# Optimization experiments

Measured on AMD Instinct MI355X. Metric: run time of the kernel, lower is better.

## Reference

```python
import jax, jax.numpy as jnp
import numpy as np

N = 100000   # num nodes
E = 1200000  # num edges
D = 64       # hidden_channel == middle_channel
ALPHA = 0.5
LN_EPS = 1e-5


def setup_inputs() -> dict:
    key = jax.random.key(0)
    ks = jax.random.split(key, 8)
    z = jax.random.normal(ks[0], (N, D), jnp.float32)
    x = jax.random.normal(ks[1], (N, D), jnp.float32)
    edge_index = jax.random.randint(ks[2], (2, E), 0, N)
    norm_factor = jax.random.uniform(ks[3], (N, 1), jnp.float32)  # >0 a.s.
    s = 0.1
    W = jax.random.normal(ks[4], (D, D), jnp.float32) * s    # nn.Linear(hidden, hidden, bias=False).weight
    U_w = jax.random.normal(ks[5], (D, D), jnp.float32) * s  # nn.Linear(hidden, middle).weight
    U_b = jax.random.normal(ks[6], (D,), jnp.float32) * s    # nn.Linear(hidden, middle).bias
    ln_gamma = jnp.ones((D,), jnp.float32)
    ln_beta = jnp.zeros((D,), jnp.float32)
    return dict(z=z, x=x, edge_index=edge_index, norm_factor=norm_factor,
                W=W, U_w=U_w, U_b=U_b, ln_gamma=ln_gamma, ln_beta=ln_beta)


def reference(z, x, edge_index, norm_factor, W, U_w, U_b, ln_gamma, ln_beta):
    row, col = edge_index[0], edge_index[1]
    # rescale=True: degree = 1/norm_factor with inf -> 0 (safe division)
    safe_nf = jnp.where(norm_factor > 0, norm_factor, 1.0)
    degree = jnp.where(norm_factor > 0, 1.0 / safe_nf, 0.0)  # [N,1]
    # double_linear=True: W(z) + degree * U(x), then graph-norm scale
    WzUx = z @ W.T + degree * (x @ U_w.T + U_b)  # [N,D]
    WzUx = norm_factor * WzUx
    # edge diff (gather), act + LayerNorm (batch=None path)
    e = WzUx[row] - WzUx[col]                    # [E,D]
    e = jax.nn.relu(e)
    mu = jnp.mean(e, axis=-1, keepdims=True)
    var = jnp.var(e, axis=-1, keepdims=True)
    e = (e - mu) * jax.lax.rsqrt(var + LN_EPS) * ln_gamma + ln_beta
    # double scatter_add aggregation
    new_z = jax.ops.segment_sum(e * norm_factor[row], row, num_segments=N)
    new_z = new_z - jax.ops.segment_sum(e * norm_factor[col], col, num_segments=N)
    # -F.linear(new_z, W.t()) == -(new_z @ W)
    new_z = -(new_z @ W)
    # dropout p=0.0 -> identity
    return ALPHA * new_z + (1.0 - ALPHA) * z
```

## Files before the change

### kernel.cpp

```cpp
#include <hip/hip_runtime.h>

#define D 64
#define LN_EPS 1e-5f
#define ALPHA 0.5f

#define GSH 8
#define GBN 256
#define NSUB 8
#define TILE 2048
#define CAPS 1280
#define CAPQ 1792
#define OVF_CAP 131072
#define MAXBUCK 400

__device__ __forceinline__ unsigned xcc_id() {
    unsigned v;
    asm volatile("s_getreg_b32 %0, hwreg(HW_REG_XCC_ID)" : "=s"(v));
    return v & (NSUB - 1);
}

__global__ __launch_bounds__(256) void wzux_kernel(
    const float* __restrict__ z, const float* __restrict__ x,
    const float* __restrict__ nf, const float* __restrict__ W,
    const float* __restrict__ Uw, const float* __restrict__ Ub,
    float* __restrict__ wzux, int N)
{
    const int lane = threadIdx.x & 63;
    const int wid  = threadIdx.x >> 6;
    const int par  = blockIdx.x & 1;
    const int half = lane >> 5;
    const int d    = par * 32 + (lane & 31);

    const float* M = half ? Uw : W;
    float4 wreg[16];
    {
        const float4* wr = (const float4*)(M + (size_t)d * D);
#pragma unroll
        for (int i = 0; i < 16; ++i) wreg[i] = wr[i];
    }
    const float ub = Ub[d];
    const float* base_src = half ? x : z;

    const int start = (blockIdx.x >> 1) * 4 + wid;
    const int step  = (gridDim.x >> 1) * 4;

    for (int n = start; n < N; n += step) {
        const int un = __builtin_amdgcn_readfirstlane(n);
        const float4* src = (const float4*)(base_src + (size_t)un * D);
        float a0 = 0.f, a1 = 0.f, a2 = 0.f, a3 = 0.f;
#pragma unroll
        for (int c = 0; c < 16; ++c) {
            float4 v = src[c];
            a0 = fmaf(v.x, wreg[c].x, a0);
            a1 = fmaf(v.y, wreg[c].y, a1);
            a2 = fmaf(v.z, wreg[c].z, a2);
            a3 = fmaf(v.w, wreg[c].w, a3);
        }
        float acc = (a0 + a1) + (a2 + a3);
        float other = __shfl_xor(acc, 32);
        if (half == 0) {
            float nfv = nf[un];
            float deg = (nfv > 0.f) ? (1.f / nfv) : 0.f;
            wzux[(size_t)un * D + d] = nfv * (acc + deg * (other + ub));
        }
    }
}

__global__ __launch_bounds__(256) void radix_scatter_kernel(
    const int* __restrict__ row, const int* __restrict__ col,
    int* __restrict__ gcur, int* __restrict__ data,
    int* __restrict__ ovf_cnt, int2* __restrict__ ovf,
    int E, int nbuck)
{
    __shared__ int cnt[MAXBUCK];
    __shared__ int gbase[MAXBUCK];
    const int t  = threadIdx.x;
    const int e0 = blockIdx.x * TILE;
    const int e1 = min(e0 + TILE, E);
    const unsigned sub = xcc_id();

    for (int i = t; i < nbuck; i += 256) cnt[i] = 0;
    __syncthreads();

    for (int e = e0 + t; e < e1; e += 256) {
        atomicAdd(&cnt[row[e] >> GSH], 1);
        atomicAdd(&cnt[col[e] >> GSH], 1);
    }
    __syncthreads();

    for (int b = t; b < nbuck; b += 256) {
        int c = cnt[b];
        gbase[b] = (c > 0) ? atomicAdd(&gcur[b * NSUB + sub], c) : 0;
    }
    __syncthreads();

    for (int e = e0 + t; e < e1; e += 256) {
        int r = row[e], c = col[e];
        {
            int b = r >> GSH;
            int s = atomicSub(&cnt[b], 1) - 1;
            int pos = gbase[b] + s;
            int rec = (c << 9) | ((r & (GBN - 1)) << 1);
            if (pos < CAPS) data[(b * NSUB + (int)sub) * CAPS + pos] = rec;
            else { int o = atomicAdd(ovf_cnt, 1);
                   if (o < OVF_CAP) ovf[o] = make_int2(b, rec); }
        }
        {
            int b = c >> GSH;
            int s = atomicSub(&cnt[b], 1) - 1;
            int pos = gbase[b] + s;
            int rec = (r << 9) | ((c & (GBN - 1)) << 1) | 1;
            if (pos < CAPS) data[(b * NSUB + (int)sub) * CAPS + pos] = rec;
            else { int o = atomicAdd(ovf_cnt, 1);
                   if (o < OVF_CAP) ovf[o] = make_int2(b, rec); }
        }
    }
}

__global__ __launch_bounds__(256) void bucket_sort_agg_kernel(
    const float4* __restrict__ wzux4,
    const int* __restrict__ gcur, const int* __restrict__ data,
    const int* __restrict__ ovf_cnt, const int2* __restrict__ ovf,
    const float* __restrict__ nf,
    const float4* __restrict__ gamma4, const float4* __restrict__ beta4,
    float4* __restrict__ out4, int N)
{
    __shared__ int sorted[CAPQ];
    __shared__ int offs[65];
    __shared__ int curs[64];

    const int blk    = blockIdx.x;
    const int base   = blk << 6;
    const int cntN   = min(64, N - base);
    const int bucket = blk >> 2;
    const int q      = blk & 3;
    const int t      = threadIdx.x;

    if (t < 65) offs[t] = 0;
    __syncthreads();

    const int ocnt = min(*ovf_cnt, OVF_CAP);

    for (int sub = 0; sub < NSUB; ++sub) {
        const int cs = min(gcur[bucket * NSUB + sub], CAPS);
        const int* p = &data[(bucket * NSUB + sub) * CAPS];
        for (int i = t; i < cs; i += 256) {
            int l8 = (p[i] >> 1) & (GBN - 1);
            if ((l8 >> 6) == q) atomicAdd(&offs[(l8 & 63) + 1], 1);
        }
    }
    for (int i = t; i < ocnt; i += 256) {
        int2 v = ovf[i];
        int l8 = (v.y >> 1) & (GBN - 1);
        if (v.x == bucket && (l8 >> 6) == q) atomicAdd(&offs[(l8 & 63) + 1], 1);
    }
    __syncthreads();

    if (t < 64) {
        int v = offs[t + 1];
#pragma unroll
        for (int off = 1; off < 64; off <<= 1) {
            int u = __shfl_up(v, off);
            if (t >= off) v += u;
        }
        offs[t + 1] = v;
    }
    __syncthreads();
    if (t < 64) curs[t] = offs[t];
    __syncthreads();

    for (int sub = 0; sub < NSUB; ++sub) {
        const int cs = min(gcur[bucket * NSUB + sub], CAPS);
        const int* p = &data[(bucket * NSUB + sub) * CAPS];
        for (int i = t; i < cs; i += 256) {
            int rec = p[i];
            int l8 = (rec >> 1) & (GBN - 1);
            if ((l8 >> 6) == q) {
                int pos = atomicAdd(&curs[l8 & 63], 1);
                if (pos < CAPQ) sorted[pos] = rec;
            }
        }
    }
    for (int i = t; i < ocnt; i += 256) {
        int2 v = ovf[i];
        int l8 = (v.y >> 1) & (GBN - 1);
        if (v.x == bucket && (l8 >> 6) == q) {
            int pos = atomicAdd(&curs[l8 & 63], 1);
            if (pos < CAPQ) sorted[pos] = v.y;
        }
    }
    __syncthreads();

    const int lane = t & 63;
    const int wid  = t >> 6;
    const int g = lane >> 4;
    const int l = lane & 15;
    const float4 gm = gamma4[l];
    const float4 bt = beta4[l];

    for (int local = wid; local < cntN; local += 4) {
        const int s = min(offs[local], CAPQ);
        const int e = min(offs[local + 1], CAPQ);
        const int n = base + local;
        const float4 self = wzux4[n * 16 + l];
        float4 acc = make_float4(0.f, 0.f, 0.f, 0.f);

#define PROC2(ENT, OROW)                                                     \
        {                                                                    \
            int ent = (ENT);                                                 \
            float sgn = (ent & 1) ? -1.f : 1.f;                              \
            float4 o = (OROW);                                               \
            float r0 = fmaxf(sgn * (self.x - o.x), 0.f);                     \
            float r1 = fmaxf(sgn * (self.y - o.y), 0.f);                     \
            float r2 = fmaxf(sgn * (self.z - o.z), 0.f);                     \
            float r3 = fmaxf(sgn * (self.w - o.w), 0.f);                     \
            float ss = r0 + r1 + r2 + r3;                                    \
            float sq = r0 * r0 + r1 * r1 + r2 * r2 + r3 * r3;                \
            _Pragma("unroll")                                                \
            for (int off = 1; off < 16; off <<= 1) {                         \
                ss += __shfl_xor(ss, off);                                   \
                sq += __shfl_xor(sq, off);                                   \
            }                                                                \
            float mu   = ss * (1.f / 64.f);                                  \
            float var  = sq * (1.f / 64.f) - mu * mu;                        \
            float rstd = rsqrtf(var + LN_EPS);                               \
            acc.x += sgn * ((r0 - mu) * rstd * gm.x + bt.x);                 \
            acc.y += sgn * ((r1 - mu) * rstd * gm.y + bt.y);                 \
            acc.z += sgn * ((r2 - mu) * rstd * gm.z + bt.z);                 \
            acc.w += sgn * ((r3 - mu) * rstd * gm.w + bt.w);                 \
        }

        int i = s + g;
        for (; i + 4 < e; i += 8) {
            int ea = sorted[i];
            int eb = sorted[i + 4];
            float4 oa = wzux4[(ea >> 9) * 16 + l];
            float4 ob = wzux4[(eb >> 9) * 16 + l];
            PROC2(ea, oa);
            PROC2(eb, ob);
        }
        if (i < e) {
            int ea = sorted[i];
            float4 oa = wzux4[(ea >> 9) * 16 + l];
            PROC2(ea, oa);
        }
#undef PROC2

#pragma unroll
        for (int m = 16; m < 64; m <<= 1) {
            acc.x += __shfl_xor(acc.x, m);
            acc.y += __shfl_xor(acc.y, m);
            acc.z += __shfl_xor(acc.z, m);
            acc.w += __shfl_xor(acc.w, m);
        }

        if (g == 0) {
            float nfv = nf[n];
            out4[n * 16 + l] = make_float4(acc.x * nfv, acc.y * nfv,
                                           acc.z * nfv, acc.w * nfv);
        }
    }
}

__global__ __launch_bounds__(256) void out_kernel(
    const float* accv, const float* __restrict__ z,
    const float* __restrict__ W, float* out, int N)
{
    const int lane = threadIdx.x & 63;
    const int wid  = threadIdx.x >> 6;

    float wcol[D];
#pragma unroll
    for (int k = 0; k < D; ++k) wcol[k] = W[k * D + lane];

    for (int n = blockIdx.x * 4 + wid; n < N; n += gridDim.x * 4) {
        const int un = __builtin_amdgcn_readfirstlane(n);
        const float4* ar = (const float4*)(accv + (size_t)un * D);
        float a0 = 0.f, a1 = 0.f, a2 = 0.f, a3 = 0.f;
#pragma unroll
        for (int c = 0; c < 16; ++c) {
            float4 a = ar[c];
            a0 = fmaf(a.x, wcol[c * 4 + 0], a0);
            a1 = fmaf(a.y, wcol[c * 4 + 1], a1);
            a2 = fmaf(a.z, wcol[c * 4 + 2], a2);
            a3 = fmaf(a.w, wcol[c * 4 + 3], a3);
        }
        float acc = (a0 + a1) + (a2 + a3);
        out[(size_t)un * D + lane] =
            (1.0f - ALPHA) * z[(size_t)un * D + lane] - ALPHA * acc;
    }
}

extern "C" void kernel_launch(void* const* d_in, const int* in_sizes, int n_in,
                              void* d_out, int out_size, void* d_ws, size_t ws_size,
                              hipStream_t stream) {
    const float* z     = (const float*)d_in[0];
    const float* x     = (const float*)d_in[1];
    const int*   ei    = (const int*)d_in[2];
    const float* nf    = (const float*)d_in[3];
    const float* W     = (const float*)d_in[4];
    const float* Uw    = (const float*)d_in[5];
    const float* Ub    = (const float*)d_in[6];
    const float* gamma = (const float*)d_in[7];
    const float* beta  = (const float*)d_in[8];

    const int N = in_sizes[0] / D;
    const int E = in_sizes[2] / 2;
    const int nbuck = (N + GBN - 1) >> GSH;

    float* out = (float*)d_out;

    char* ws = (char*)d_ws;
    size_t off = 0;
    auto alloc = [&](size_t bytes) {
        char* p = ws + off;
        off += (bytes + 255) & ~(size_t)255;
        return p;
    };
    float* wzux    = (float*)alloc((size_t)N * D * sizeof(float));
    int*   gcur    = (int*)  alloc((size_t)nbuck * NSUB * sizeof(int));
    int*   ovf_cnt = (int*)  alloc(sizeof(int));
    int*   data    = (int*)  alloc((size_t)nbuck * NSUB * CAPS * sizeof(int));
    int2*  ovf     = (int2*) alloc((size_t)OVF_CAP * sizeof(int2));

    hipMemsetAsync(gcur, 0, (size_t)nbuck * NSUB * sizeof(int), stream);
    hipMemsetAsync(ovf_cnt, 0, sizeof(int), stream);

    wzux_kernel<<<2048, 256, 0, stream>>>(z, x, nf, W, Uw, Ub, wzux, N);

    int sb = (E + TILE - 1) / TILE;
    radix_scatter_kernel<<<sb, 256, 0, stream>>>(ei, ei + E, gcur, data,
                                                 ovf_cnt, ovf, E, nbuck);

    int ab = (N + 63) / 64;
    bucket_sort_agg_kernel<<<ab, 256, 0, stream>>>(
        (const float4*)wzux, gcur, data, ovf_cnt, ovf, nf,
        (const float4*)gamma, (const float4*)beta,
        (float4*)out, N);

    out_kernel<<<2048, 256, 0, stream>>>(out, z, W, out, N);
}
```

Before: 341.4 us.

## Merge independent front kernels and fuse output GEMV into aggregation

The wzux linear-projection kernel and the radix edge-scatter kernel are independent, so they are merged into one launch, with block ranges dispatched to each role so both run concurrently. The final out_kernel (new_z @ W plus residual) is fused into the aggregation kernel. Each wave stages its reduced row in shared memory and computes the 64x64 matvec with W columns held in registers. This removes two launches and a global round trip of the intermediate row, at the cost of 64 extra registers per thread in the aggregation kernel, which may lower occupancy.

```diff
diff --git a/kernel.cpp b/kernel.cpp
--- a/kernel.cpp
+++ b/kernel.cpp
@@ -12,6 +12,7 @@
 #define CAPQ 1792
 #define OVF_CAP 131072
 #define MAXBUCK 400
+#define WZB 2048
 
 __device__ __forceinline__ unsigned xcc_id() {
     unsigned v;
@@ -19,100 +20,101 @@
     return v & (NSUB - 1);
 }
 
-__global__ __launch_bounds__(256) void wzux_kernel(
+__global__ __launch_bounds__(256) void front_kernel(
+    const int* __restrict__ row, const int* __restrict__ col,
+    int* __restrict__ gcur, int* __restrict__ data,
+    int* __restrict__ ovf_cnt, int2* __restrict__ ovf,
+    int E, int nbuck, int sb,
     const float* __restrict__ z, const float* __restrict__ x,
     const float* __restrict__ nf, const float* __restrict__ W,
     const float* __restrict__ Uw, const float* __restrict__ Ub,
     float* __restrict__ wzux, int N)
 {
-    const int lane = threadIdx.x & 63;
-    const int wid  = threadIdx.x >> 6;
-    const int par  = blockIdx.x & 1;
-    const int half = lane >> 5;
-    const int d    = par * 32 + (lane & 31);
-
-    const float* M = half ? Uw : W;
-    float4 wreg[16];
-    {
-        const float4* wr = (const float4*)(M + (size_t)d * D);
-#pragma unroll
-        for (int i = 0; i < 16; ++i) wreg[i] = wr[i];
-    }
-    const float ub = Ub[d];
-    const float* base_src = half ? x : z;
-
-    const int start = (blockIdx.x >> 1) * 4 + wid;
-    const int step  = (gridDim.x >> 1) * 4;
-
-    for (int n = start; n < N; n += step) {
-        const int un = __builtin_amdgcn_readfirstlane(n);
-        const float4* src = (const float4*)(base_src + (size_t)un * D);
-        float a0 = 0.f, a1 = 0.f, a2 = 0.f, a3 = 0.f;
-#pragma unroll
-        for (int c = 0; c < 16; ++c) {
-            float4 v = src[c];
-            a0 = fmaf(v.x, wreg[c].x, a0);
-            a1 = fmaf(v.y, wreg[c].y, a1);
-            a2 = fmaf(v.z, wreg[c].z, a2);
-            a3 = fmaf(v.w, wreg[c].w, a3);
-        }
-        float acc = (a0 + a1) + (a2 + a3);
-        float other = __shfl_xor(acc, 32);
-        if (half == 0) {
-            float nfv = nf[un];
-            float deg = (nfv > 0.f) ? (1.f / nfv) : 0.f;
-            wzux[(size_t)un * D + d] = nfv * (acc + deg * (other + ub));
-        }
-    }
-}
-
-__global__ __launch_bounds__(256) void radix_scatter_kernel(
-    const int* __restrict__ row, const int* __restrict__ col,
-    int* __restrict__ gcur, int* __restrict__ data,
-    int* __restrict__ ovf_cnt, int2* __restrict__ ovf,
-    int E, int nbuck)
-{
     __shared__ int cnt[MAXBUCK];
     __shared__ int gbase[MAXBUCK];
-    const int t  = threadIdx.x;
-    const int e0 = blockIdx.x * TILE;
-    const int e1 = min(e0 + TILE, E);
-    const unsigned sub = xcc_id();
-
-    for (int i = t; i < nbuck; i += 256) cnt[i] = 0;
-    __syncthreads();
-
-    for (int e = e0 + t; e < e1; e += 256) {
-        atomicAdd(&cnt[row[e] >> GSH], 1);
-        atomicAdd(&cnt[col[e] >> GSH], 1);
-    }
-    __syncthreads();
-
-    for (int b = t; b < nbuck; b += 256) {
-        int c = cnt[b];
-        gbase[b] = (c > 0) ? atomicAdd(&gcur[b * NSUB + sub], c) : 0;
-    }
-    __syncthreads();
-
-    for (int e = e0 + t; e < e1; e += 256) {
-        int r = row[e], c = col[e];
+    const int t = threadIdx.x;
+
+    if ((int)blockIdx.x < sb) {
+        const int e0 = blockIdx.x * TILE;
+        const int e1 = min(e0 + TILE, E);
+        const unsigned sub = xcc_id();
+
+        for (int i = t; i < nbuck; i += 256) cnt[i] = 0;
+        __syncthreads();
+
+        for (int e = e0 + t; e < e1; e += 256) {
+            atomicAdd(&cnt[row[e] >> GSH], 1);
+            atomicAdd(&cnt[col[e] >> GSH], 1);
+        }
+        __syncthreads();
+
+        for (int b = t; b < nbuck; b += 256) {
+            int c = cnt[b];
+            gbase[b] = (c > 0) ? atomicAdd(&gcur[b * NSUB + sub], c) : 0;
+        }
+        __syncthreads();
+
+        for (int e = e0 + t; e < e1; e += 256) {
+            int r = row[e], c = col[e];
+            {
+                int b = r >> GSH;
+                int s = atomicSub(&cnt[b], 1) - 1;
+                int pos = gbase[b] + s;
+                int rec = (c << 9) | ((r & (GBN - 1)) << 1);
+                if (pos < CAPS) data[(b * NSUB + (int)sub) * CAPS + pos] = rec;
+                else { int o = atomicAdd(ovf_cnt, 1);
+                       if (o < OVF_CAP) ovf[o] = make_int2(b, rec); }
+            }
+            {
+                int b = c >> GSH;
+                int s = atomicSub(&cnt[b], 1) - 1;
+                int pos = gbase[b] + s;
+                int rec = (r << 9) | ((c & (GBN - 1)) << 1) | 1;
+                if (pos < CAPS) data[(b * NSUB + (int)sub) * CAPS + pos] = rec;
+                else { int o = atomicAdd(ovf_cnt, 1);
+                       if (o < OVF_CAP) ovf[o] = make_int2(b, rec); }
+            }
+        }
+    } else {
+        const int wb   = blockIdx.x - sb;
+        const int lane = t & 63;
+        const int wid  = t >> 6;
+        const int par  = wb & 1;
+        const int half = lane >> 5;
+        const int d    = par * 32 + (lane & 31);
+
+        const float* M = half ? Uw : W;
+        float4 wreg[16];
         {
-            int b = r >> GSH;
-            int s = atomicSub(&cnt[b], 1) - 1;
-            int pos = gbase[b] + s;
-            int rec = (c << 9) | ((r & (GBN - 1)) << 1);
-            if (pos < CAPS) data[(b * NSUB + (int)sub) * CAPS + pos] = rec;
-            else { int o = atomicAdd(ovf_cnt, 1);
-                   if (o < OVF_CAP) ovf[o] = make_int2(b, rec); }
-        }
-        {
-            int b = c >> GSH;
-            int s = atomicSub(&cnt[b], 1) - 1;
-            int pos = gbase[b] + s;
-            int rec = (r << 9) | ((c & (GBN - 1)) << 1) | 1;
-            if (pos < CAPS) data[(b * NSUB + (int)sub) * CAPS + pos] = rec;
-            else { int o = atomicAdd(ovf_cnt, 1);
-                   if (o < OVF_CAP) ovf[o] = make_int2(b, rec); }
+            const float4* wr = (const float4*)(M + (size_t)d * D);
+#pragma unroll
+            for (int i = 0; i < 16; ++i) wreg[i] = wr[i];
+        }
+        const float ub = Ub[d];
+        const float* base_src = half ? x : z;
+
+        const int start = (wb >> 1) * 4 + wid;
+        const int step  = (WZB >> 1) * 4;
+
+        for (int n = start; n < N; n += step) {
+            const int un = __builtin_amdgcn_readfirstlane(n);
+            const float4* src = (const float4*)(base_src + (size_t)un * D);
+            float a0 = 0.f, a1 = 0.f, a2 = 0.f, a3 = 0.f;
+#pragma unroll
+            for (int c = 0; c < 16; ++c) {
+                float4 v = src[c];
+                a0 = fmaf(v.x, wreg[c].x, a0);
+                a1 = fmaf(v.y, wreg[c].y, a1);
+                a2 = fmaf(v.z, wreg[c].z, a2);
+                a3 = fmaf(v.w, wreg[c].w, a3);
+            }
+            float acc = (a0 + a1) + (a2 + a3);
+            float other = __shfl_xor(acc, 32);
+            if (half == 0) {
+                float nfv = nf[un];
+                float deg = (nfv > 0.f) ? (1.f / nfv) : 0.f;
+                wzux[(size_t)un * D + d] = nfv * (acc + deg * (other + ub));
+            }
         }
     }
 }
@@ -123,11 +125,13 @@
     const int* __restrict__ ovf_cnt, const int2* __restrict__ ovf,
     const float* __restrict__ nf,
     const float4* __restrict__ gamma4, const float4* __restrict__ beta4,
-    float4* __restrict__ out4, int N)
+    const float* __restrict__ z, const float* __restrict__ W,
+    float* __restrict__ out, int N)
 {
     __shared__ int sorted[CAPQ];
     __shared__ int offs[65];
     __shared__ int curs[64];
+    __shared__ float4 rowbuf[4][17];
 
     const int blk    = blockIdx.x;
     const int base   = blk << 6;
@@ -135,6 +139,12 @@
     const int bucket = blk >> 2;
     const int q      = blk & 3;
     const int t      = threadIdx.x;
+    const int lane   = t & 63;
+    const int wid    = t >> 6;
+
+    float wcol[D];
+#pragma unroll
+    for (int k = 0; k < D; ++k) wcol[k] = W[k * D + lane];
 
     if (t < 65) offs[t] = 0;
     __syncthreads();
@@ -191,8 +201,6 @@
     }
     __syncthreads();
 
-    const int lane = t & 63;
-    const int wid  = t >> 6;
     const int g = lane >> 4;
     const int l = lane & 15;
     const float4 gm = gamma4[l];
@@ -254,40 +262,23 @@
             acc.w += __shfl_xor(acc.w, m);
         }
 
+        float nfv = nf[n];
         if (g == 0) {
-            float nfv = nf[n];
-            out4[n * 16 + l] = make_float4(acc.x * nfv, acc.y * nfv,
-                                           acc.z * nfv, acc.w * nfv);
-        }
-    }
-}
-
-__global__ __launch_bounds__(256) void out_kernel(
-    const float* accv, const float* __restrict__ z,
-    const float* __restrict__ W, float* out, int N)
-{
-    const int lane = threadIdx.x & 63;
-    const int wid  = threadIdx.x >> 6;
-
-    float wcol[D];
-#pragma unroll
-    for (int k = 0; k < D; ++k) wcol[k] = W[k * D + lane];
-
-    for (int n = blockIdx.x * 4 + wid; n < N; n += gridDim.x * 4) {
-        const int un = __builtin_amdgcn_readfirstlane(n);
-        const float4* ar = (const float4*)(accv + (size_t)un * D);
-        float a0 = 0.f, a1 = 0.f, a2 = 0.f, a3 = 0.f;
+            rowbuf[wid][l] = make_float4(acc.x * nfv, acc.y * nfv,
+                                         acc.z * nfv, acc.w * nfv);
+        }
+        float m0 = 0.f, m1 = 0.f, m2 = 0.f, m3 = 0.f;
 #pragma unroll
         for (int c = 0; c < 16; ++c) {
-            float4 a = ar[c];
-            a0 = fmaf(a.x, wcol[c * 4 + 0], a0);
-            a1 = fmaf(a.y, wcol[c * 4 + 1], a1);
-            a2 = fmaf(a.z, wcol[c * 4 + 2], a2);
-            a3 = fmaf(a.w, wcol[c * 4 + 3], a3);
-        }
-        float acc = (a0 + a1) + (a2 + a3);
-        out[(size_t)un * D + lane] =
-            (1.0f - ALPHA) * z[(size_t)un * D + lane] - ALPHA * acc;
+            float4 rv = rowbuf[wid][c];
+            m0 = fmaf(rv.x, wcol[c * 4 + 0], m0);
+            m1 = fmaf(rv.y, wcol[c * 4 + 1], m1);
+            m2 = fmaf(rv.z, wcol[c * 4 + 2], m2);
+            m3 = fmaf(rv.w, wcol[c * 4 + 3], m3);
+        }
+        out[(size_t)n * D + lane] =
+            (1.0f - ALPHA) * z[(size_t)n * D + lane]
+            - ALPHA * ((m0 + m1) + (m2 + m3));
     }
 }
 
@@ -307,6 +298,7 @@
     const int N = in_sizes[0] / D;
     const int E = in_sizes[2] / 2;
     const int nbuck = (N + GBN - 1) >> GSH;
+    const int sb = (E + TILE - 1) / TILE;
 
     float* out = (float*)d_out;
 
@@ -326,17 +318,13 @@
     hipMemsetAsync(gcur, 0, (size_t)nbuck * NSUB * sizeof(int), stream);
     hipMemsetAsync(ovf_cnt, 0, sizeof(int), stream);
 
-    wzux_kernel<<<2048, 256, 0, stream>>>(z, x, nf, W, Uw, Ub, wzux, N);
-
-    int sb = (E + TILE - 1) / TILE;
-    radix_scatter_kernel<<<sb, 256, 0, stream>>>(ei, ei + E, gcur, data,
-                                                 ovf_cnt, ovf, E, nbuck);
+    front_kernel<<<sb + WZB, 256, 0, stream>>>(
+        ei, ei + E, gcur, data, ovf_cnt, ovf, E, nbuck, sb,
+        z, x, nf, W, Uw, Ub, wzux, N);
 
     int ab = (N + 63) / 64;
     bucket_sort_agg_kernel<<<ab, 256, 0, stream>>>(
         (const float4*)wzux, gcur, data, ovf_cnt, ovf, nf,
         (const float4*)gamma, (const float4*)beta,
-        (float4*)out, N);
-
-    out_kernel<<<2048, 256, 0, stream>>>(out, z, W, out, N);
+        z, W, out, N);
 }
```

Result: faster. 322.5 us (-5.5%).

## Store WzUx in bf16, fuse projection with radix scatter, unroll gather by four

Applied to the files above, without the earlier changes.

The intermediate WzUx table is now stored as bf16, which halves the bytes moved by the per-edge random gathers in the aggregation kernel. The dense projection and the edge radix scatter become one launch, split by block index, so the two independent phases run concurrently and one kernel launch is saved. The gather loop now issues four row loads per iteration instead of two, for more memory-level parallelism. The risk is bf16 rounding error feeding into the LayerNorm differences, which could break accuracy tolerance.

```diff
diff --git a/kernel.cpp b/kernel.cpp
--- a/kernel.cpp
+++ b/kernel.cpp
@@ -12,6 +12,7 @@
 #define CAPQ 1792
 #define OVF_CAP 131072
 #define MAXBUCK 400
+#define WZB 2048
 
 __device__ __forceinline__ unsigned xcc_id() {
     unsigned v;
@@ -19,106 +20,116 @@
     return v & (NSUB - 1);
 }
 
-__global__ __launch_bounds__(256) void wzux_kernel(
+__device__ __forceinline__ unsigned short f2bf(float f) {
+    unsigned u = __float_as_uint(f);
+    u += 0x7FFF + ((u >> 16) & 1);
+    return (unsigned short)(u >> 16);
+}
+__device__ __forceinline__ float bf2f(unsigned short h) {
+    return __uint_as_float(((unsigned)h) << 16);
+}
+
+__global__ __launch_bounds__(256) void front_kernel(
+    const int* __restrict__ row, const int* __restrict__ col,
+    int* __restrict__ gcur, int* __restrict__ data,
+    int* __restrict__ ovf_cnt, int2* __restrict__ ovf,
+    int E, int nbuck, int sb,
     const float* __restrict__ z, const float* __restrict__ x,
     const float* __restrict__ nf, const float* __restrict__ W,
     const float* __restrict__ Uw, const float* __restrict__ Ub,
-    float* __restrict__ wzux, int N)
-{
-    const int lane = threadIdx.x & 63;
-    const int wid  = threadIdx.x >> 6;
-    const int par  = blockIdx.x & 1;
-    const int half = lane >> 5;
-    const int d    = par * 32 + (lane & 31);
-
-    const float* M = half ? Uw : W;
-    float4 wreg[16];
-    {
-        const float4* wr = (const float4*)(M + (size_t)d * D);
-#pragma unroll
-        for (int i = 0; i < 16; ++i) wreg[i] = wr[i];
-    }
-    const float ub = Ub[d];
-    const float* base_src = half ? x : z;
-
-    const int start = (blockIdx.x >> 1) * 4 + wid;
-    const int step  = (gridDim.x >> 1) * 4;
-
-    for (int n = start; n < N; n += step) {
-        const int un = __builtin_amdgcn_readfirstlane(n);
-        const float4* src = (const float4*)(base_src + (size_t)un * D);
-        float a0 = 0.f, a1 = 0.f, a2 = 0.f, a3 = 0.f;
-#pragma unroll
-        for (int c = 0; c < 16; ++c) {
-            float4 v = src[c];
-            a0 = fmaf(v.x, wreg[c].x, a0);
-            a1 = fmaf(v.y, wreg[c].y, a1);
-            a2 = fmaf(v.z, wreg[c].z, a2);
-            a3 = fmaf(v.w, wreg[c].w, a3);
-        }
-        float acc = (a0 + a1) + (a2 + a3);
-        float other = __shfl_xor(acc, 32);
-        if (half == 0) {
-            float nfv = nf[un];
-            float deg = (nfv > 0.f) ? (1.f / nfv) : 0.f;
-            wzux[(size_t)un * D + d] = nfv * (acc + deg * (other + ub));
-        }
-    }
-}
-
-__global__ __launch_bounds__(256) void radix_scatter_kernel(
-    const int* __restrict__ row, const int* __restrict__ col,
-    int* __restrict__ gcur, int* __restrict__ data,
-    int* __restrict__ ovf_cnt, int2* __restrict__ ovf,
-    int E, int nbuck)
+    unsigned short* __restrict__ wzux, int N)
 {
     __shared__ int cnt[MAXBUCK];
     __shared__ int gbase[MAXBUCK];
-    const int t  = threadIdx.x;
-    const int e0 = blockIdx.x * TILE;
-    const int e1 = min(e0 + TILE, E);
-    const unsigned sub = xcc_id();
-
-    for (int i = t; i < nbuck; i += 256) cnt[i] = 0;
-    __syncthreads();
-
-    for (int e = e0 + t; e < e1; e += 256) {
-        atomicAdd(&cnt[row[e] >> GSH], 1);
-        atomicAdd(&cnt[col[e] >> GSH], 1);
-    }
-    __syncthreads();
-
-    for (int b = t; b < nbuck; b += 256) {
-        int c = cnt[b];
-        gbase[b] = (c > 0) ? atomicAdd(&gcur[b * NSUB + sub], c) : 0;
-    }
-    __syncthreads();
-
-    for (int e = e0 + t; e < e1; e += 256) {
-        int r = row[e], c = col[e];
+    const int t = threadIdx.x;
+
+    if ((int)blockIdx.x < sb) {
+        const int e0 = blockIdx.x * TILE;
+        const int e1 = min(e0 + TILE, E);
+        const unsigned sub = xcc_id();
+
+        for (int i = t; i < nbuck; i += 256) cnt[i] = 0;
+        __syncthreads();
+
+        for (int e = e0 + t; e < e1; e += 256) {
+            atomicAdd(&cnt[row[e] >> GSH], 1);
+            atomicAdd(&cnt[col[e] >> GSH], 1);
+        }
+        __syncthreads();
+
+        for (int b = t; b < nbuck; b += 256) {
+            int c = cnt[b];
+            gbase[b] = (c > 0) ? atomicAdd(&gcur[b * NSUB + sub], c) : 0;
+        }
+        __syncthreads();
+
+        for (int e = e0 + t; e < e1; e += 256) {
+            int r = row[e], c = col[e];
+            {
+                int b = r >> GSH;
+                int s = atomicSub(&cnt[b], 1) - 1;
+                int pos = gbase[b] + s;
+                int rec = (c << 9) | ((r & (GBN - 1)) << 1);
+                if (pos < CAPS) data[(b * NSUB + (int)sub) * CAPS + pos] = rec;
+                else { int o = atomicAdd(ovf_cnt, 1);
+                       if (o < OVF_CAP) ovf[o] = make_int2(b, rec); }
+            }
+            {
+                int b = c >> GSH;
+                int s = atomicSub(&cnt[b], 1) - 1;
+                int pos = gbase[b] + s;
+                int rec = (r << 9) | ((c & (GBN - 1)) << 1) | 1;
+                if (pos < CAPS) data[(b * NSUB + (int)sub) * CAPS + pos] = rec;
+                else { int o = atomicAdd(ovf_cnt, 1);
+                       if (o < OVF_CAP) ovf[o] = make_int2(b, rec); }
+            }
+        }
+    } else {
+        const int wb   = blockIdx.x - sb;
+        const int lane = t & 63;
+        const int wid  = t >> 6;
+        const int par  = wb & 1;
+        const int half = lane >> 5;
+        const int d    = par * 32 + (lane & 31);
+
+        const float* M = half ? Uw : W;
+        float4 wreg[16];
         {
-            int b = r >> GSH;
-            int s = atomicSub(&cnt[b], 1) - 1;
-            int pos = gbase[b] + s;
-            int rec = (c << 9) | ((r & (GBN - 1)) << 1);
-            if (pos < CAPS) data[(b * NSUB + (int)sub) * CAPS + pos] = rec;
-            else { int o = atomicAdd(ovf_cnt, 1);
-                   if (o < OVF_CAP) ovf[o] = make_int2(b, rec); }
-        }
-        {
-            int b = c >> GSH;
-            int s = atomicSub(&cnt[b], 1) - 1;
-            int pos = gbase[b] + s;
-            int rec = (r << 9) | ((c & (GBN - 1)) << 1) | 1;
-            if (pos < CAPS) data[(b * NSUB + (int)sub) * CAPS + pos] = rec;
-            else { int o = atomicAdd(ovf_cnt, 1);
-                   if (o < OVF_CAP) ovf[o] = make_int2(b, rec); }
+            const float4* wr = (const float4*)(M + (size_t)d * D);
+#pragma unroll
+            for (int i = 0; i < 16; ++i) wreg[i] = wr[i];
+        }
+        const float ub = Ub[d];
+        const float* base_src = half ? x : z;
+
+        const int start = (wb >> 1) * 4 + wid;
+        const int step  = (WZB >> 1) * 4;
+
+        for (int n = start; n < N; n += step) {
+            const int un = __builtin_amdgcn_readfirstlane(n);
+            const float4* src = (const float4*)(base_src + (size_t)un * D);
+            float a0 = 0.f, a1 = 0.f, a2 = 0.f, a3 = 0.f;
+#pragma unroll
+            for (int c = 0; c < 16; ++c) {
+                float4 v = src[c];
+                a0 = fmaf(v.x, wreg[c].x, a0);
+                a1 = fmaf(v.y, wreg[c].y, a1);
+                a2 = fmaf(v.z, wreg[c].z, a2);
+                a3 = fmaf(v.w, wreg[c].w, a3);
+            }
+            float acc = (a0 + a1) + (a2 + a3);
+            float other = __shfl_xor(acc, 32);
+            if (half == 0) {
+                float nfv = nf[un];
+                float deg = (nfv > 0.f) ? (1.f / nfv) : 0.f;
+                wzux[(size_t)un * D + d] = f2bf(nfv * (acc + deg * (other + ub)));
+            }
         }
     }
 }
 
 __global__ __launch_bounds__(256) void bucket_sort_agg_kernel(
-    const float4* __restrict__ wzux4,
+    const unsigned short* __restrict__ wzux,
     const int* __restrict__ gcur, const int* __restrict__ data,
     const int* __restrict__ ovf_cnt, const int2* __restrict__ ovf,
     const float* __restrict__ nf,
@@ -197,19 +208,23 @@
     const int l = lane & 15;
     const float4 gm = gamma4[l];
     const float4 bt = beta4[l];
+    const ushort4* wz4 = (const ushort4*)wzux;
 
     for (int local = wid; local < cntN; local += 4) {
         const int s = min(offs[local], CAPQ);
         const int e = min(offs[local + 1], CAPQ);
         const int n = base + local;
-        const float4 self = wzux4[n * 16 + l];
+        ushort4 sh = wz4[n * 16 + l];
+        const float4 self = make_float4(bf2f(sh.x), bf2f(sh.y),
+                                        bf2f(sh.z), bf2f(sh.w));
         float4 acc = make_float4(0.f, 0.f, 0.f, 0.f);
 
-#define PROC2(ENT, OROW)                                                     \
+#define PROC2(ENT, H)                                                        \
         {                                                                    \
             int ent = (ENT);                                                 \
             float sgn = (ent & 1) ? -1.f : 1.f;                              \
-            float4 o = (OROW);                                               \
+            float4 o = make_float4(bf2f((H).x), bf2f((H).y),                 \
+                                   bf2f((H).z), bf2f((H).w));                \
             float r0 = fmaxf(sgn * (self.x - o.x), 0.f);                     \
             float r1 = fmaxf(sgn * (self.y - o.y), 0.f);                     \
             float r2 = fmaxf(sgn * (self.z - o.z), 0.f);                     \
@@ -231,18 +246,24 @@
         }
 
         int i = s + g;
-        for (; i + 4 < e; i += 8) {
-            int ea = sorted[i];
-            int eb = sorted[i + 4];
-            float4 oa = wzux4[(ea >> 9) * 16 + l];
-            float4 ob = wzux4[(eb >> 9) * 16 + l];
-            PROC2(ea, oa);
-            PROC2(eb, ob);
-        }
-        if (i < e) {
-            int ea = sorted[i];
-            float4 oa = wzux4[(ea >> 9) * 16 + l];
-            PROC2(ea, oa);
+        for (; i + 12 < e; i += 16) {
+            int e0 = sorted[i];
+            int e1 = sorted[i + 4];
+            int e2 = sorted[i + 8];
+            int e3 = sorted[i + 12];
+            ushort4 h0 = wz4[(e0 >> 9) * 16 + l];
+            ushort4 h1 = wz4[(e1 >> 9) * 16 + l];
+            ushort4 h2 = wz4[(e2 >> 9) * 16 + l];
+            ushort4 h3 = wz4[(e3 >> 9) * 16 + l];
+            PROC2(e0, h0);
+            PROC2(e1, h1);
+            PROC2(e2, h2);
+            PROC2(e3, h3);
+        }
+        for (; i < e; i += 4) {
+            int e0 = sorted[i];
+            ushort4 h0 = wz4[(e0 >> 9) * 16 + l];
+            PROC2(e0, h0);
         }
 #undef PROC2
 
@@ -307,6 +328,7 @@
     const int N = in_sizes[0] / D;
     const int E = in_sizes[2] / 2;
     const int nbuck = (N + GBN - 1) >> GSH;
+    const int sb = (E + TILE - 1) / TILE;
 
     float* out = (float*)d_out;
 
@@ -317,7 +339,7 @@
         off += (bytes + 255) & ~(size_t)255;
         return p;
     };
-    float* wzux    = (float*)alloc((size_t)N * D * sizeof(float));
+    unsigned short* wzux = (unsigned short*)alloc((size_t)N * D * 2);
     int*   gcur    = (int*)  alloc((size_t)nbuck * NSUB * sizeof(int));
     int*   ovf_cnt = (int*)  alloc(sizeof(int));
     int*   data    = (int*)  alloc((size_t)nbuck * NSUB * CAPS * sizeof(int));
@@ -326,15 +348,13 @@
     hipMemsetAsync(gcur, 0, (size_t)nbuck * NSUB * sizeof(int), stream);
     hipMemsetAsync(ovf_cnt, 0, sizeof(int), stream);
 
-    wzux_kernel<<<2048, 256, 0, stream>>>(z, x, nf, W, Uw, Ub, wzux, N);
-
-    int sb = (E + TILE - 1) / TILE;
-    radix_scatter_kernel<<<sb, 256, 0, stream>>>(ei, ei + E, gcur, data,
-                                                 ovf_cnt, ovf, E, nbuck);
+    front_kernel<<<sb + WZB, 256, 0, stream>>>(
+        ei, ei + E, gcur, data, ovf_cnt, ovf, E, nbuck, sb,
+        z, x, nf, W, Uw, Ub, wzux, N);
 
     int ab = (N + 63) / 64;
     bucket_sort_agg_kernel<<<ab, 256, 0, stream>>>(
-        (const float4*)wzux, gcur, data, ovf_cnt, ovf, nf,
+        wzux, gcur, data, ovf_cnt, ovf, nf,
         (const float4*)gamma, (const float4*)beta,
         (float4*)out, N);
 
```

After: 340.2 us. No clear change (-0.3%).
